# Optimization experiments

Hardware: AMD Instinct MI355X
Metric: run time of the kernel (lower is better)

## Reference

```python
import jax, jax.numpy as jnp
import numpy as np

V, E, Hd, ENC, A = 2000, 256, 256, 256, 256
B, HI, WI, T = 64, 16, 32, 256


def setup_inputs() -> dict:
    key = jax.random.key(0)
    ks = jax.random.split(key, 24)
    n = lambda k, s: jax.random.normal(k, s, dtype=jnp.float32) * 0.05
    return {
        "encoder_out": jax.random.normal(ks[0], (B, ENC, HI, WI), dtype=jnp.float32),
        "captions": jax.random.randint(ks[1], (B, T), 0, V),
        "emb": n(ks[2], (V, E)),
        "W_ae": n(ks[3], (A, ENC)), "b_ae": jnp.zeros((A,), jnp.float32),
        "W_ad": n(ks[4], (A, Hd)), "b_ad": jnp.zeros((A,), jnp.float32),
        "W_fa": n(ks[5], (1, A)), "b_fa": jnp.zeros((1,), jnp.float32),
        "W_inith": n(ks[6], (Hd, ENC)), "b_inith": jnp.zeros((Hd,), jnp.float32),
        "W_initc": n(ks[7], (Hd, ENC)), "b_initc": jnp.zeros((Hd,), jnp.float32),
        "W_ih0": n(ks[8], (4 * Hd, E + ENC)), "W_hh0": n(ks[9], (4 * Hd, Hd)),
        "b_ih0": jnp.zeros((4 * Hd,), jnp.float32), "b_hh0": jnp.zeros((4 * Hd,), jnp.float32),
        "W_ih1": n(ks[10], (4 * Hd, Hd)), "W_hh1": n(ks[11], (4 * Hd, Hd)),
        "b_ih1": jnp.zeros((4 * Hd,), jnp.float32), "b_hh1": jnp.zeros((4 * Hd,), jnp.float32),
        "W_out": n(ks[12], (V, Hd)), "b_out": jnp.zeros((V,), jnp.float32),
    }


def _lstm_cell(x, h, c, Wih, Whh, bih, bhh):
    # PyTorch LSTM gate order: i, f, g, o
    g = x @ Wih.T + h @ Whh.T + bih + bhh
    i, f, gg, o = jnp.split(g, 4, axis=-1)
    c2 = jax.nn.sigmoid(f) * c + jax.nn.sigmoid(i) * jnp.tanh(gg)
    h2 = jax.nn.sigmoid(o) * jnp.tanh(c2)
    return h2, c2


def reference(encoder_out, captions, emb, W_ae, b_ae, W_ad, b_ad, W_fa, b_fa,
              W_inith, b_inith, W_initc, b_initc,
              W_ih0, W_hh0, b_ih0, b_hh0, W_ih1, W_hh1, b_ih1, b_hh1,
              W_out, b_out):
    Bsz, C = encoder_out.shape[0], encoder_out.shape[1]
    enc = encoder_out.reshape(Bsz, C, -1).transpose(0, 2, 1)  # [B, P, C]
    mean = encoder_out.mean(axis=(2, 3))                      # [B, C]
    h0 = jnp.tanh(mean @ W_inith.T + b_inith)
    c0 = jnp.tanh(mean @ W_initc.T + b_initc)
    h = jnp.stack([h0, h0])  # [L, B, Hd]
    c = jnp.stack([c0, c0])
    embs = emb[captions]     # [B, T, E] (dropout disabled / eval)
    att1 = enc @ W_ae.T + b_ae  # [B, P, A], hoisted out of the loop (same math)

    def step(carry, e_t):
        h, c = carry
        att2 = h[-1] @ W_ad.T + b_ad                              # [B, A]
        score = (jnp.tanh(att1 + att2[:, None, :]) @ W_fa.T)[..., 0] + b_fa[0]  # [B, P]
        w = jax.nn.softmax(score, axis=1)
        ctx = jnp.einsum('bp,bpc->bc', w, enc)
        x = jnp.concatenate([e_t, ctx], axis=1)                   # [B, E+C]
        h0n, c0n = _lstm_cell(x, h[0], c[0], W_ih0, W_hh0, b_ih0, b_hh0)
        h1n, c1n = _lstm_cell(h0n, h[1], c[1], W_ih1, W_hh1, b_ih1, b_hh1)
        out_t = h1n @ W_out.T + b_out
        return (jnp.stack([h0n, h1n]), jnp.stack([c0n, c1n])), (out_t, w)

    _, (outs, ws) = jax.lax.scan(step, (h, c), embs.transpose(1, 0, 2))
    return outs.transpose(1, 0, 2), ws.transpose(1, 0, 2)  # [B,T,V], [B,T,P]
```

## Files before the change

kernel.cpp:

```cpp
#include <hip/hip_runtime.h>
#include <math.h>

#define BB 64
#define TT 256
#define VV 2000
#define EE 256
#define HD 256
#define ENC 256
#define AA 256
#define PP 512

#define S2L 2.8853900817779268f
#define SL  1.4426950408889634f


typedef unsigned uvec4 __attribute__((ext_vector_type(4)));

__device__ __forceinline__ unsigned short f2h(float f) {
    _Float16 h = (_Float16)f; return __builtin_bit_cast(unsigned short, h);
}
__device__ __forceinline__ void fmlo(float& a, unsigned w, float x) {
    asm("v_fma_mix_f32 %0, %1, %2, %0 op_sel_hi:[1,0,0]" : "+v"(a) : "v"(w), "v"(x));
}
__device__ __forceinline__ void fmhi(float& a, unsigned w, float x) {
    asm("v_fma_mix_f32 %0, %1, %2, %0 op_sel:[1,0,0] op_sel_hi:[1,0,0]" : "+v"(a) : "v"(w), "v"(x));
}
__device__ __forceinline__ void dot8m(float& a0, float& a1, uvec4 w, float4 xa, float4 xb) {
    fmlo(a0, w.x, xa.x); fmhi(a1, w.x, xa.y);
    fmlo(a0, w.y, xa.z); fmhi(a1, w.y, xa.w);
    fmlo(a0, w.z, xb.x); fmhi(a1, w.z, xb.y);
    fmlo(a0, w.w, xb.z); fmhi(a1, w.w, xb.w);
}
__device__ __forceinline__ void dot8s(float& a, uvec4 w, const float* x) {
    fmlo(a, w.x, x[0]); fmhi(a, w.x, x[1]);
    fmlo(a, w.y, x[2]); fmhi(a, w.y, x[3]);
    fmlo(a, w.z, x[4]); fmhi(a, w.z, x[5]);
    fmlo(a, w.w, x[6]); fmhi(a, w.w, x[7]);
}
__device__ __forceinline__ float ftanh(float x) {
    float u = __builtin_amdgcn_exp2f(x * S2L);
    return 1.f - 2.f * __builtin_amdgcn_rcpf(u + 1.f);
}
__device__ __forceinline__ float fsigm(float x) {
    float u = __builtin_amdgcn_exp2f(x * SL);
    return u * __builtin_amdgcn_rcpf(u + 1.f);
}


__global__ void k_mean(const float* __restrict__ enc, float* __restrict__ meanb) {
    int b = blockIdx.x, c = threadIdx.x;
    const float4* p4 = reinterpret_cast<const float4*>(enc + ((size_t)b*ENC + c)*PP);
    float s = 0.f;
    for (int i = 0; i < PP/4; ++i) { float4 v = p4[i]; s += v.x + v.y + v.z + v.w; }
    meanb[b*ENC + c] = s * (1.0f/PP);
}

__global__ void k_init(const float* __restrict__ meanb,
                       const float* __restrict__ Winith, const float* __restrict__ binith,
                       const float* __restrict__ Winitc, const float* __restrict__ binitc,
                       float* __restrict__ h0, float* __restrict__ c0,
                       float* __restrict__ h1i, float* __restrict__ c1) {
    __shared__ float ms[ENC];
    int b = blockIdx.x, j = threadIdx.x;
    ms[j] = meanb[b*ENC + j];
    __syncthreads();
    float ah = binith[j], ac = binitc[j];
    const float4* wh = (const float4*)(Winith + (size_t)j*ENC);
    const float4* wc = (const float4*)(Winitc + (size_t)j*ENC);
    const float4* m4 = (const float4*)ms;
    for (int k = 0; k < ENC/4; ++k) {
        float4 m = m4[k], a = wh[k], b2 = wc[k];
        ah += a.x*m.x + a.y*m.y + a.z*m.z + a.w*m.w;
        ac += b2.x*m.x + b2.y*m.y + b2.z*m.z + b2.w*m.w;
    }
    float hv = tanhf(ah), cv = tanhf(ac);
    h0[b*HD + j] = hv; c0[b*HD + j] = cv;
    h1i[b*HD + j] = hv; c1[b*HD + j] = cv;
}

__global__ void k_att1T8(const float* __restrict__ enc, const float* __restrict__ Wae,
                         const float* __restrict__ bae, unsigned short* __restrict__ att1T8) {
    __shared__ float wsm[16][ENC];
    int a0 = blockIdx.x * 16, b = blockIdx.y, p = threadIdx.x;
    for (int i = threadIdx.x; i < 16*ENC; i += 512) wsm[i >> 8][i & 255] = Wae[(size_t)a0*ENC + i];
    __syncthreads();
    float acc[16];
    #pragma unroll
    for (int i = 0; i < 16; ++i) acc[i] = 0.f;
    const float* eb = enc + (size_t)b*ENC*PP + p;
    for (int c = 0; c < ENC; ++c) {
        float v = eb[(size_t)c*PP];
        #pragma unroll
        for (int i = 0; i < 16; ++i) acc[i] += v * wsm[i][c];
    }
    #pragma unroll
    for (int q = 0; q < 2; ++q) {
        unsigned short o[8];
        #pragma unroll
        for (int j = 0; j < 8; ++j) o[j] = f2h((acc[q*8+j] + bae[a0 + q*8 + j]) * S2L);
        *(uint4*)(att1T8 + (((size_t)b*32 + (a0 >> 3) + q)*PP + p)*8) = *(const uint4*)o;
    }
}

__global__ void k_encP(const float* __restrict__ enc, unsigned short* __restrict__ encP) {
    __shared__ float tile[256*33];
    int b = blockIdx.x, p0 = blockIdx.y * 32, tid = threadIdx.x;
    for (int i = tid; i < 256*32; i += 256) {
        int c = i >> 5, pl = i & 31;
        tile[c*33 + pl] = enc[((size_t)b*ENC + c)*PP + p0 + pl];
    }
    __syncthreads();
    for (int j = tid; j < 32*256; j += 256) {
        int p = j >> 8, c = j & 255;
        encP[((size_t)b*PP + p0 + p)*ENC + c] = f2h(tile[c*33 + p]);
    }
}

__global__ void k_cvtT8(const float* __restrict__ src, unsigned short* __restrict__ dst,
                        int nsh, int kc, float scale) {
    int i = blockIdx.x*256 + threadIdx.x;
    int N = 1 << nsh;
    int kk = i >> nsh, n = i & (N - 1);
    const float* s = src + (size_t)n*(kc*8) + kk*8;
    unsigned short o[8];
    #pragma unroll
    for (int j = 0; j < 8; ++j) o[j] = f2h(s[j] * scale);
    *(uint4*)(dst + ((size_t)kk*N + n)*8) = *(const uint4*)o;
}

__global__ void k_cvtW(const float* __restrict__ src, unsigned short* __restrict__ dst) {
    int i = blockIdx.x*256 + threadIdx.x;
    int kk = i >> 11, v = i & 2047;
    unsigned short o[8] = {0,0,0,0,0,0,0,0};
    if (v < VV) {
        const float* s = src + (size_t)v*HD + kk*8;
        #pragma unroll
        for (int j = 0; j < 8; ++j) o[j] = f2h(s[j]);
    }
    *(uint4*)(dst + ((size_t)kk*2048 + v)*8) = *(const uint4*)o;
}

__global__ __launch_bounds__(1024) void k_E(const int* __restrict__ caps,
                                            const float* __restrict__ emb,
                                            const unsigned short* __restrict__ Wih0T8,
                                            unsigned short* __restrict__ E) {
    __shared__ float xs[16][256];
    __shared__ int cp[16];
    int b = blockIdx.x, tc = blockIdx.y, tid = threadIdx.x;
    if (tid < 16) cp[tid] = caps[b*TT + tc*16 + tid];
    __syncthreads();
    for (int i = tid; i < 16*256; i += 1024) {
        int r = i >> 8, c = i & 255;
        xs[r][c] = emb[(size_t)cp[r]*EE + c];
    }
    __syncthreads();
    const uvec4* wt = (const uvec4*)Wih0T8;
    float acc[16];
    #pragma unroll
    for (int r = 0; r < 16; ++r) acc[r] = 0.f;
    for (int kk = 0; kk < 32; ++kk) {
        uvec4 w = wt[(size_t)kk*1024 + tid];
        #pragma unroll
        for (int r = 0; r < 16; ++r) dot8s(acc[r], w, &xs[r][kk*8]);
    }
    #pragma unroll
    for (int r = 0; r < 16; ++r)
        E[((size_t)(b*TT + tc*16 + r))*1024 + tid] = f2h(acc[r]);
}


struct KP2 {
    const int* caps; const float* emb;
    const float* Wfa; const float* bfa; const float* bad;
    const float* bih0; const float* bhh0; const float* bih1; const float* bhh1;
    const unsigned short* WadT8;
    const unsigned short* Wih0T8;
    const unsigned short* Whh0T8;
    const unsigned short* Wih1T8;
    const unsigned short* Whh1T8;
    const unsigned short* att1T8;
    const unsigned short* encP;
    const unsigned short* E;
    const float* h0g; const float* c0g; const float* h1g; const float* c1g;
    float* H1all; float* wsout;
};

template <int USEE>
__global__ __launch_bounds__(1024, 1) void main64(KP2 P) {
    __shared__ float att2s[AA];
    __shared__ float xt[512];
    __shared__ float h0s[HD], h1s[HD];
    __shared__ float es[PP];
    __shared__ float red[2048];
    __shared__ float bs0[1024], bs1[1024];
    __shared__ float badS[AA], wfaS[AA];
    __shared__ float zinvS, bfaS, wfaSumS;

    const int b = blockIdx.x, tid = threadIdx.x;

    bs0[tid] = P.bih0[tid] + P.bhh0[tid];
    bs1[tid] = P.bih1[tid] + P.bhh1[tid];
    float c0r = 0.f, c1r = 0.f;
    if (tid < 256) {
        badS[tid] = P.bad[tid] * S2L;
        wfaS[tid] = P.Wfa[tid] * SL;
        h0s[tid] = P.h0g[b*HD + tid]; h1s[tid] = P.h1g[b*HD + tid];
        c0r = P.c0g[b*HD + tid];      c1r = P.c1g[b*HD + tid];
    }
    if (tid == 0) bfaS = P.bfa[0] * SL;
    __syncthreads();
    if (tid == 0) {
        float s = 0.f;
        for (int i = 0; i < 256; ++i) s += wfaS[i];
        wfaSumS = s;
    }
    __syncthreads();

    const int p_sc = tid & 511, h_sc = tid >> 9;
    const uvec4* att1b = (const uvec4*)(P.att1T8 + (size_t)b*32*PP*8) + (size_t)(h_sc*16)*PP + p_sc;
    const unsigned short* Eb = P.E + (size_t)b*TT*1024;
    const unsigned* encPb = (const unsigned*)(P.encP + (size_t)b*PP*ENC);
    const uvec4* wadt = (const uvec4*)P.WadT8;
    const uvec4* wi0t = (const uvec4*)P.Wih0T8;
    const uvec4* wh0t = (const uvec4*)P.Whh0T8;
    const uvec4* wi1t = (const uvec4*)P.Wih1T8;
    const uvec4* wh1t = (const uvec4*)P.Whh1T8;

    for (int t = 0; t < TT; ++t) {
        {
            int a = tid & 255, kq = tid >> 8;
            const uvec4* w4 = wadt + (size_t)(kq*8)*256 + a;
            const float4* hv = (const float4*)h1s;
            float a0 = 0.f, a1 = 0.f;
            #pragma unroll
            for (int i = 0; i < 8; ++i) {
                uvec4 w = w4[(size_t)i*256];
                dot8m(a0, a1, w, hv[(kq*8 + i)*2], hv[(kq*8 + i)*2 + 1]);
            }
            red[kq*256 + a] = a0 + a1;
        }
        if (!USEE && tid < 256) {
            int cap = P.caps[b*TT + t];
            xt[tid] = P.emb[(size_t)cap*EE + tid];
        }
        __syncthreads();
        if (tid < 256) att2s[tid] = red[tid] + red[256+tid] + red[512+tid] + red[768+tid] + badS[tid];
        __syncthreads();

        {
            float partial = 0.f;
            #pragma unroll 4
            for (int i = 0; i < 16; ++i) {
                uvec4 w = __builtin_nontemporal_load(att1b + (size_t)i*PP);
                int ab = (h_sc*16 + i)*8;
                #pragma unroll
                for (int j = 0; j < 4; ++j) {
                    unsigned wj = w[j];
                    float a2l = att2s[ab + j*2], a2h = att2s[ab + j*2 + 1];
                    float x0, x1;
                    asm("v_fma_mix_f32 %0, %1, %2, %3 op_sel_hi:[1,0,0]"
                        : "=v"(x0) : "v"(wj), "v"(1.0f), "v"(a2l));
                    asm("v_fma_mix_f32 %0, %1, %2, %3 op_sel:[1,0,0] op_sel_hi:[1,0,0]"
                        : "=v"(x1) : "v"(wj), "v"(1.0f), "v"(a2h));
                    float r0 = __builtin_amdgcn_rcpf(__builtin_amdgcn_exp2f(x0) + 1.f);
                    float r1 = __builtin_amdgcn_rcpf(__builtin_amdgcn_exp2f(x1) + 1.f);
                    partial = fmaf(wfaS[ab + j*2],     r0, partial);
                    partial = fmaf(wfaS[ab + j*2 + 1], r1, partial);
                }
            }
            red[h_sc*512 + p_sc] = partial;
        }
        __syncthreads();
        if (tid < 512)
            es[tid] = __builtin_amdgcn_exp2f(wfaSumS - 2.f*(red[tid] + red[512 + tid]) + bfaS);
        __syncthreads();

        if (tid < 64) {
            float z = 0.f;
            #pragma unroll
            for (int i = 0; i < 8; ++i) z += es[tid*8 + i];
            for (int o = 32; o > 0; o >>= 1) z += __shfl_down(z, o, 64);
            if (tid == 0) zinvS = 1.f / z;
        }
        {
            int c2 = tid & 127, pq = tid >> 7;
            float a0 = 0.f, a1 = 0.f;
            #pragma unroll 8
            for (int i = 0; i < 64; ++i) {
                int p = pq*64 + i;
                unsigned w = __builtin_nontemporal_load(encPb + (size_t)p*128 + c2);
                float e = es[p];
                fmlo(a0, w, e); fmhi(a1, w, e);
            }
            red[pq*256 + c2*2]     = a0;
            red[pq*256 + c2*2 + 1] = a1;
        }
        __syncthreads();
        if (tid < 256) {
            float s = 0.f;
            #pragma unroll
            for (int q = 0; q < 8; ++q) s += red[q*256 + tid];
            xt[256 + tid] = s * zinvS;
        } else if (tid >= 512) {
            int p = tid - 512;
            P.wsout[((size_t)b*TT + t)*PP + p] = es[p] * zinvS;
        }
        __syncthreads();

        {
            float a0 = bs0[tid], a1 = 0.f;
            if (USEE) {
                unsigned short eu = Eb[(size_t)t*1024 + tid];
                a0 += (float)__builtin_bit_cast(_Float16, eu);
            }
            const uvec4* wi = wi0t + tid;
            const float4* xv = (const float4*)xt;
            if (USEE) {
                #pragma unroll 8
                for (int kk = 32; kk < 64; ++kk) {
                    uvec4 w = wi[(size_t)kk*1024];
                    dot8m(a0, a1, w, xv[kk*2], xv[kk*2 + 1]);
                }
            } else {
                #pragma unroll 8
                for (int kk = 0; kk < 64; ++kk) {
                    uvec4 w = wi[(size_t)kk*1024];
                    dot8m(a0, a1, w, xv[kk*2], xv[kk*2 + 1]);
                }
            }
            const uvec4* wh = wh0t + tid;
            const float4* hv = (const float4*)h0s;
            #pragma unroll 8
            for (int kk = 0; kk < 32; ++kk) {
                uvec4 w = wh[(size_t)kk*1024];
                dot8m(a0, a1, w, hv[kk*2], hv[kk*2 + 1]);
            }
            red[tid] = a0 + a1;
        }
        __syncthreads();
        if (tid < 256) {
            float gi = red[tid], gf = red[HD+tid], gg = red[2*HD+tid], go = red[3*HD+tid];
            c0r = fsigm(gf)*c0r + fsigm(gi)*ftanh(gg);
            h0s[tid] = fsigm(go)*ftanh(c0r);
        }
        __syncthreads();

        {
            float a0 = bs1[tid], a1 = 0.f;
            const uvec4* wi = wi1t + tid;
            const float4* hv0 = (const float4*)h0s;
            #pragma unroll 8
            for (int kk = 0; kk < 32; ++kk) {
                uvec4 w = wi[(size_t)kk*1024];
                dot8m(a0, a1, w, hv0[kk*2], hv0[kk*2 + 1]);
            }
            const uvec4* wh = wh1t + tid;
            const float4* hv1 = (const float4*)h1s;
            #pragma unroll 8
            for (int kk = 0; kk < 32; ++kk) {
                uvec4 w = wh[(size_t)kk*1024];
                dot8m(a0, a1, w, hv1[kk*2], hv1[kk*2 + 1]);
            }
            red[tid] = a0 + a1;
        }
        __syncthreads();
        if (tid < 256) {
            float gi = red[tid], gf = red[HD+tid], gg = red[2*HD+tid], go = red[3*HD+tid];
            c1r = fsigm(gf)*c1r + fsigm(gi)*ftanh(gg);
            float h = fsigm(go)*ftanh(c1r);
            h1s[tid] = h;
            P.H1all[((size_t)t*BB + b)*HD + tid] = h;
        }
        __syncthreads();
    }
}


__global__ __launch_bounds__(256)
void f2o(const float* __restrict__ H1all, const unsigned short* __restrict__ WoT8,
         const float* __restrict__ bout, float* __restrict__ out0) {
    int vt = blockIdx.x, rt = blockIdx.y, tid = threadIdx.x;
    int v = vt*256 + tid;
    const float* Hrow = H1all + (size_t)rt*32*HD;
    const uvec4* wt = (const uvec4*)WoT8;
    float acc[32];
    #pragma unroll
    for (int r = 0; r < 32; ++r) acc[r] = 0.f;
    for (int kk = 0; kk < 32; ++kk) {
        uvec4 w = wt[(size_t)kk*2048 + v];
        #pragma unroll
        for (int r = 0; r < 32; ++r) dot8s(acc[r], w, Hrow + r*HD + kk*8);
    }
    if (v < VV) {
        float bv = bout[v];
        #pragma unroll
        for (int r = 0; r < 32; ++r) {
            int row = rt*32 + r, tt = row >> 6, bb = row & 63;
            out0[((size_t)bb*TT + tt)*VV + v] = acc[r] + bv;
        }
    }
}


extern "C" void kernel_launch(void* const* d_in, const int* in_sizes, int n_in,
                              void* d_out, int out_size, void* d_ws, size_t ws_size,
                              hipStream_t stream) {
    const float* enc    = (const float*)d_in[0];
    const int*   caps   = (const int*)  d_in[1];
    const float* emb    = (const float*)d_in[2];
    const float* Wae    = (const float*)d_in[3];
    const float* bae    = (const float*)d_in[4];
    const float* Wad    = (const float*)d_in[5];
    const float* bad    = (const float*)d_in[6];
    const float* Wfa    = (const float*)d_in[7];
    const float* bfa    = (const float*)d_in[8];
    const float* Winith = (const float*)d_in[9];
    const float* binith = (const float*)d_in[10];
    const float* Winitc = (const float*)d_in[11];
    const float* binitc = (const float*)d_in[12];
    const float* Wih0   = (const float*)d_in[13];
    const float* Whh0   = (const float*)d_in[14];
    const float* bih0   = (const float*)d_in[15];
    const float* bhh0   = (const float*)d_in[16];
    const float* Wih1   = (const float*)d_in[17];
    const float* Whh1   = (const float*)d_in[18];
    const float* bih1   = (const float*)d_in[19];
    const float* bhh1   = (const float*)d_in[20];
    const float* Wout   = (const float*)d_in[21];
    const float* bout   = (const float*)d_in[22];

    float* ws = (float*)d_ws;
    unsigned short* att1T8 = (unsigned short*)(ws);
    unsigned short* encP   = (unsigned short*)(ws + 4194304);
    float* H1all = ws + 8388608;
    unsigned short* Wih0T8 = (unsigned short*)(ws + 12582912);
    unsigned short* Whh0T8 = (unsigned short*)(ws + 12845056);
    unsigned short* Wih1T8 = (unsigned short*)(ws + 12976128);
    unsigned short* Whh1T8 = (unsigned short*)(ws + 13107200);
    unsigned short* WadT8  = (unsigned short*)(ws + 13238272);
    float* meanb = ws + 13271040;
    float* h0g   = ws + 13287424;
    float* c0g   = ws + 13303808;
    float* h1g   = ws + 13320192;
    float* c1g   = ws + 13336576;
    unsigned short* E = (unsigned short*)(ws + 13352960);

    const int useE = (ws_size >= (size_t)(13352960 + 8388608) * 4) ? 1 : 0;
    const int useWtail = (ws_size >= (size_t)(13352960 + 8388608 + 262144) * 4) ? 1 : 0;
    unsigned short* WoT8 = useWtail ? (unsigned short*)(ws + 13352960 + 8388608)
                                    : att1T8;

    float* out0  = (float*)d_out;
    float* wsout = out0 + (size_t)BB*TT*VV;

    hipLaunchKernelGGL(k_mean,   dim3(BB),     dim3(256), 0, stream, enc, meanb);
    hipLaunchKernelGGL(k_init,   dim3(BB),     dim3(256), 0, stream, meanb, Winith, binith,
                       Winitc, binitc, h0g, c0g, h1g, c1g);
    hipLaunchKernelGGL(k_att1T8, dim3(16, BB), dim3(512), 0, stream, enc, Wae, bae, att1T8);
    hipLaunchKernelGGL(k_encP,   dim3(BB, 16), dim3(256), 0, stream, enc, encP);
    hipLaunchKernelGGL(k_cvtT8,  dim3(256),    dim3(256), 0, stream, Wih0, Wih0T8, 10, 64, 1.0f);
    hipLaunchKernelGGL(k_cvtT8,  dim3(128),    dim3(256), 0, stream, Whh0, Whh0T8, 10, 32, 1.0f);
    hipLaunchKernelGGL(k_cvtT8,  dim3(128),    dim3(256), 0, stream, Wih1, Wih1T8, 10, 32, 1.0f);
    hipLaunchKernelGGL(k_cvtT8,  dim3(128),    dim3(256), 0, stream, Whh1, Whh1T8, 10, 32, 1.0f);
    hipLaunchKernelGGL(k_cvtT8,  dim3(32),     dim3(256), 0, stream, Wad,  WadT8,   8, 32, S2L);
    if (useE)
        hipLaunchKernelGGL(k_E,  dim3(BB, 16), dim3(1024), 0, stream, caps, emb, Wih0T8, E);
    if (useWtail)
        hipLaunchKernelGGL(k_cvtW, dim3(256),  dim3(256), 0, stream, Wout, WoT8);

    KP2 kp;
    kp.caps = caps; kp.emb = emb;
    kp.Wfa = Wfa; kp.bfa = bfa; kp.bad = bad;
    kp.bih0 = bih0; kp.bhh0 = bhh0; kp.bih1 = bih1; kp.bhh1 = bhh1;
    kp.WadT8 = WadT8; kp.Wih0T8 = Wih0T8; kp.Whh0T8 = Whh0T8; kp.Wih1T8 = Wih1T8; kp.Whh1T8 = Whh1T8;
    kp.att1T8 = att1T8; kp.encP = encP; kp.E = E;
    kp.h0g = h0g; kp.c0g = c0g; kp.h1g = h1g; kp.c1g = c1g;
    kp.H1all = H1all; kp.wsout = wsout;

    if (useE)
        hipLaunchKernelGGL((main64<1>), dim3(BB), dim3(1024), 0, stream, kp);
    else
        hipLaunchKernelGGL((main64<0>), dim3(BB), dim3(1024), 0, stream, kp);

    if (!useWtail)
        hipLaunchKernelGGL(k_cvtW, dim3(256),  dim3(256), 0, stream, Wout, WoT8);

    hipLaunchKernelGGL(f2o, dim3(8, 512), dim3(256), 0, stream, H1all, WoT8, bout, out0);
}
```

Baseline: 10.10 ms.

## Overlap layer-1 recurrent matvec with attention scoring via warp specialization

Attention scoring now runs on only 512 threads, each covering all 32 attention chunks, and the exp is written to es directly, which removes one reduction barrier. The other 512 threads compute the layer-1 W_hh·h1 gate contribution into new shared memory during the scoring phase. That work depends only on the previous h1, so it no longer has to be computed after the layer-0 LSTM step. The cost is a longer serial loop per scoring thread and a larger shared-memory footprint.

```diff
diff --git a/kernel.cpp b/kernel.cpp
--- a/kernel.cpp
+++ b/kernel.cpp
@@ -192,6 +192,7 @@
     __shared__ float h0s[HD], h1s[HD];
     __shared__ float es[PP];
     __shared__ float red[2048];
+    __shared__ float gh1s[1024];
     __shared__ float bs0[1024], bs1[1024];
     __shared__ float badS[AA], wfaS[AA];
     __shared__ float zinvS, bfaS, wfaSumS;
@@ -216,8 +217,8 @@
     }
     __syncthreads();
 
-    const int p_sc = tid & 511, h_sc = tid >> 9;
-    const uvec4* att1b = (const uvec4*)(P.att1T8 + (size_t)b*32*PP*8) + (size_t)(h_sc*16)*PP + p_sc;
+    const int p_sc = tid & 511;
+    const uvec4* att1b = (const uvec4*)(P.att1T8 + (size_t)b*32*PP*8) + p_sc;
     const unsigned short* Eb = P.E + (size_t)b*TT*1024;
     const unsigned* encPb = (const unsigned*)(P.encP + (size_t)b*PP*ENC);
     const uvec4* wadt = (const uvec4*)P.WadT8;
@@ -247,12 +248,12 @@
         if (tid < 256) att2s[tid] = red[tid] + red[256+tid] + red[512+tid] + red[768+tid] + badS[tid];
         __syncthreads();
 
-        {
+        if (tid < 512) {
             float partial = 0.f;
             #pragma unroll 4
-            for (int i = 0; i < 16; ++i) {
+            for (int i = 0; i < 32; ++i) {
                 uvec4 w = __builtin_nontemporal_load(att1b + (size_t)i*PP);
-                int ab = (h_sc*16 + i)*8;
+                int ab = i*8;
                 #pragma unroll
                 for (int j = 0; j < 4; ++j) {
                     unsigned wj = w[j];
@@ -268,11 +269,24 @@
                     partial = fmaf(wfaS[ab + j*2 + 1], r1, partial);
                 }
             }
-            red[h_sc*512 + p_sc] = partial;
-        }
-        __syncthreads();
-        if (tid < 512)
-            es[tid] = __builtin_amdgcn_exp2f(wfaSumS - 2.f*(red[tid] + red[512 + tid]) + bfaS);
+            es[p_sc] = __builtin_amdgcn_exp2f(wfaSumS - 2.f*partial + bfaS);
+        } else {
+            int g2 = tid - 512;
+            const uvec4* wA = wh1t + g2;
+            const uvec4* wB = wh1t + g2 + 512;
+            const float4* hv1 = (const float4*)h1s;
+            float sA0 = 0.f, sA1 = 0.f, sB0 = 0.f, sB1 = 0.f;
+            #pragma unroll 8
+            for (int kk = 0; kk < 32; ++kk) {
+                uvec4 wa = wA[(size_t)kk*1024];
+                uvec4 wb = wB[(size_t)kk*1024];
+                float4 ha = hv1[kk*2], hb = hv1[kk*2 + 1];
+                dot8m(sA0, sA1, wa, ha, hb);
+                dot8m(sB0, sB1, wb, ha, hb);
+            }
+            gh1s[g2]       = sA0 + sA1;
+            gh1s[g2 + 512] = sB0 + sB1;
+        }
         __syncthreads();
 
         if (tid < 64) {
@@ -346,20 +360,13 @@
         __syncthreads();
 
         {
-            float a0 = bs1[tid], a1 = 0.f;
+            float a0 = bs1[tid] + gh1s[tid], a1 = 0.f;
             const uvec4* wi = wi1t + tid;
             const float4* hv0 = (const float4*)h0s;
             #pragma unroll 8
             for (int kk = 0; kk < 32; ++kk) {
                 uvec4 w = wi[(size_t)kk*1024];
                 dot8m(a0, a1, w, hv0[kk*2], hv0[kk*2 + 1]);
-            }
-            const uvec4* wh = wh1t + tid;
-            const float4* hv1 = (const float4*)h1s;
-            #pragma unroll 8
-            for (int kk = 0; kk < 32; ++kk) {
-                uvec4 w = wh[(size_t)kk*1024];
-                dot8m(a0, a1, w, hv1[kk*2], hv1[kk*2 + 1]);
             }
             red[tid] = a0 + a1;
         }
```

Measured after the change: 11.08 ms. 9.7% more time.
